# Kernel optimization log

Measured on AMD Instinct MI355X. Metric: run time of the kernel, lower is better.

The kernel has to match this reference:

```python
import jax, jax.numpy as jnp
import numpy as np

N = 131072      # 8192 sudoku puzzles x 16 cells
E = 1048576     # random constraint edges (avg degree 8)
HID = 64
NEG_SLOPE = 0.2


def setup_inputs() -> dict:
    key = jax.random.key(0)
    ks = jax.random.split(key, 18)
    p = lambda k, shape: jax.random.normal(k, shape, dtype=jnp.float32) * 0.05
    return {
        "x": jax.random.randint(ks[0], (N,), 0, 5),
        "edge_index": jax.random.randint(ks[1], (2, E), 0, N),
        "emb": p(ks[2], (5, HID)),
        # conv1: in 64 -> heads=4, C=64, concat
        "W1": p(ks[3], (HID, 4 * HID)),
        "a1_src": p(ks[4], (4, HID)),
        "a1_dst": p(ks[5], (4, HID)),
        "b1": p(ks[6], (4 * HID,)),
        # conv2: in 256 -> heads=4, C=64, concat
        "W2": p(ks[7], (4 * HID, 4 * HID)),
        "a2_src": p(ks[8], (4, HID)),
        "a2_dst": p(ks[9], (4, HID)),
        "b2": p(ks[10], (4 * HID,)),
        # conv3: in 256 -> heads=1, C=64, no concat
        "W3": p(ks[11], (4 * HID, HID)),
        "a3_src": p(ks[12], (1, HID)),
        "a3_dst": p(ks[13], (1, HID)),
        "b3": p(ks[14], (HID,)),
        "fc_w": p(ks[15], (HID, 5)),
        "fc_b": p(ks[16], (5,)),
    }


def gat_conv(x, src, dst, W, a_src, a_dst, b, concat):
    """PyG-style GATConv (self-loops already appended to src/dst)."""
    n = x.shape[0]
    H, C = a_src.shape
    h = (x @ W).reshape(n, H, C)                       # [N,H,C]
    alpha_s = jnp.einsum('nhc,hc->nh', h, a_src)       # [N,H]
    alpha_d = jnp.einsum('nhc,hc->nh', h, a_dst)
    e = jax.nn.leaky_relu(alpha_s[src] + alpha_d[dst], NEG_SLOPE)  # [E,H]
    # scatter-softmax over incoming edges per destination node
    e_max = jax.ops.segment_max(e, dst, num_segments=n)
    e_exp = jnp.exp(e - e_max[dst])
    denom = jax.ops.segment_sum(e_exp, dst, num_segments=n)
    alpha = e_exp / (denom[dst] + 1e-16)               # [E,H]
    msg = h[src] * alpha[:, :, None]                   # [E,H,C]
    out = jax.ops.segment_sum(msg, dst, num_segments=n)  # [N,H,C]
    out = out.reshape(n, H * C) if concat else out.mean(axis=1)
    return out + b


def reference(x, edge_index, emb, W1, a1_src, a1_dst, b1,
              W2, a2_src, a2_dst, b2, W3, a3_src, a3_dst, b3, fc_w, fc_b):
    n = x.shape[0]
    loops = jnp.arange(n)
    src = jnp.concatenate([edge_index[0], loops])  # add self-loops (PyG default)
    dst = jnp.concatenate([edge_index[1], loops])
    h = emb[x]                                                    # [N,64]
    h = jax.nn.elu(gat_conv(h, src, dst, W1, a1_src, a1_dst, b1, True))
    h = jax.nn.elu(gat_conv(h, src, dst, W2, a2_src, a2_dst, b2, True))
    h = jax.nn.elu(gat_conv(h, src, dst, W3, a3_src, a3_dst, b3, False))
    return h @ fc_w + fc_b                                        # [N,5]
```

## Files before the change

### kernel.cpp

```cpp
#include <hip/hip_runtime.h>
#include <hip/hip_bf16.h>
#include <hip/hip_fp8.h>

typedef __attribute__((ext_vector_type(8))) short short8;
typedef __attribute__((ext_vector_type(4))) short short4_t;
typedef __attribute__((ext_vector_type(4))) float floatx4;
typedef __attribute__((ext_vector_type(2))) float floatx2;

constexpr int NB  = 256;
constexpr int CAP = 6144;

__device__ __forceinline__ unsigned short f2bf(float f){
  unsigned int u = __float_as_uint(f);
  u += 0x7FFF + ((u >> 16) & 1);
  return (unsigned short)(u >> 16);
}
__device__ __forceinline__ float bf2f(unsigned short h){
  return __uint_as_float(((unsigned int)h) << 16);
}
__device__ __forceinline__ float lrelu(float x){ return x > 0.f ? x : 0.2f * x; }
__device__ __forceinline__ float eluf(float x){ return x > 0.f ? x : (__expf(x) - 1.f); }

__device__ __forceinline__ unsigned char f2fp8(float f){
  __hip_fp8_e4m3 t(f);
  return (unsigned char)t.__x;
}
__device__ __forceinline__ float fp82f(unsigned char b){
  __hip_fp8_e4m3 t;
  t.__x = (__hip_fp8_storage_t)b;
  return (float)t;
}

template<bool HI>
__device__ __forceinline__ floatx2 fp8pk2(unsigned int v){
#if defined(__has_builtin) && __has_builtin(__builtin_amdgcn_cvt_pk_f32_fp8)
  return __builtin_amdgcn_cvt_pk_f32_fp8((int)v, HI);
#else
  floatx2 r;
  constexpr int sh = HI ? 16 : 0;
  r.x = fp82f((unsigned char)((v >> sh) & 0xFF));
  r.y = fp82f((unsigned char)((v >> (sh + 8)) & 0xFF));
  return r;
#endif
}

__device__ __forceinline__ unsigned int f32x4_to_fp8(float a0, float a1, float a2, float a3){
#if defined(__has_builtin) && __has_builtin(__builtin_amdgcn_cvt_pk_fp8_f32)
  int w = 0;
  w = __builtin_amdgcn_cvt_pk_fp8_f32(a0, a1, w, false);
  w = __builtin_amdgcn_cvt_pk_fp8_f32(a2, a3, w, true);
  return (unsigned int)w;
#else
  return (unsigned int)f2fp8(a0) | ((unsigned int)f2fp8(a1) << 8) |
         ((unsigned int)f2fp8(a2) << 16) | ((unsigned int)f2fp8(a3) << 24);
#endif
}

__device__ __forceinline__ void gload16(const unsigned short* g, unsigned short* l){
  __builtin_amdgcn_global_load_lds(
      (const __attribute__((address_space(1))) unsigned int*)(const void*)g,
      (__attribute__((address_space(3))) unsigned int*)(void*)l,
      16, 0, 0);
}

__global__ __launch_bounds__(256) void part_prep_k(const int* __restrict__ ei, int E, int shift,
                                                   int* __restrict__ gcnt,
                                                   uint2* __restrict__ bbuf, int PB,
                                                   const float* __restrict__ W2,
                                                   unsigned short* __restrict__ Wp2,
                                                   const float* __restrict__ W3,
                                                   unsigned short* __restrict__ Wp3,
                                                   const float* __restrict__ emb,
                                                   const float* __restrict__ W1,
                                                   const float* __restrict__ a1s,
                                                   const float* __restrict__ a1d,
                                                   float* __restrict__ T1,
                                                   float* __restrict__ wt_tab){
  int blk = blockIdx.x;
  int tid = threadIdx.x;
  if (blk < PB){
    __shared__ int hist[NB];
    __shared__ int base[NB];
    hist[tid] = 0;
    __syncthreads();
    int blk_start = blk * 4096;
    int src[16], bkt[16], lp[16];
    #pragma unroll
    for (int k = 0; k < 16; k++){
      int i = blk_start + k * 256 + tid;
      if (i < E){
        int dst = ei[E + i];
        src[k] = ei[i];
        bkt[k] = dst >> shift;
        lp[k] = atomicAdd(&hist[bkt[k]], 1);
      } else {
        bkt[k] = -1;
      }
    }
    __syncthreads();
    base[tid] = atomicAdd(&gcnt[tid], hist[tid]);
    __syncthreads();
    #pragma unroll
    for (int k = 0; k < 16; k++){
      int i = blk_start + k * 256 + tid;
      if (i < E){
        int b = bkt[k];
        int dst = ei[E + i];
        bbuf[(size_t)b * CAP + base[b] + lp[k]] = make_uint2((unsigned)src[k], (unsigned)dst);
      }
    }
    return;
  }
  int b = blk - PB;
  if (b < 256){
    int idx = b * 256 + tid;
    int k = idx >> 8, nn = idx & 255;
    Wp2[nn * 256 + k] = f2bf(W2[idx]);
  } else if (b < 320){
    int idx = (b - 256) * 256 + tid;
    int k = idx >> 6, nn = idx & 63;
    Wp3[nn * 256 + k] = f2bf(W3[idx]);
  } else {
    __shared__ float t_lds[1280];
    __shared__ float as_l[20], ad_l[20];
    for (int i = tid; i < 1280; i += 256){
      int r = i >> 8, c = i & 255;
      float s = 0.f;
      for (int k = 0; k < 64; k++) s += emb[r * 64 + k] * W1[k * 256 + c];
      t_lds[i] = s;
      T1[i] = s;
    }
    __syncthreads();
    if (tid < 20){
      int r = tid >> 2, hh = tid & 3;
      float ss = 0.f, sd = 0.f;
      for (int c = 0; c < 64; c++){
        float f = t_lds[r * 256 + hh * 64 + c];
        ss += f * a1s[hh * 64 + c];
        sd += f * a1d[hh * 64 + c];
      }
      as_l[tid] = ss;
      ad_l[tid] = sd;
    }
    __syncthreads();
    if (tid < 100){
      int xd = tid / 20, rest = tid % 20;
      int h = rest & 3;
      wt_tab[tid] = __expf(lrelu(as_l[rest] + ad_l[xd * 4 + h]));
    }
  }
}

__global__ __launch_bounds__(256) void bscan_k(const int* __restrict__ gcnt,
                                               int* __restrict__ gbase,
                                               int* __restrict__ row_ptr, int N, int dpb){
  __shared__ int s[NB];
  int t = threadIdx.x;
  int v = gcnt[t] + dpb;
  s[t] = v;
  __syncthreads();
  #pragma unroll
  for (int off = 1; off < NB; off <<= 1){
    int u = (t >= off) ? s[t - off] : 0;
    __syncthreads();
    s[t] += u;
    __syncthreads();
  }
  gbase[t] = s[t] - v;
  if (t == NB - 1){ gbase[NB] = s[t]; row_ptr[N] = s[t]; }
}

__global__ __launch_bounds__(256) void sort_k(const uint2* __restrict__ bbuf,
                                              const int* __restrict__ gcnt,
                                              const int* __restrict__ gbase,
                                              int* __restrict__ row_ptr,
                                              int* __restrict__ sorted_src, int dpb){
  __shared__ int counts[512];
  __shared__ int curs[512];
  __shared__ int wsum[256];
  __shared__ int sortedL[CAP + 512];
  int b = blockIdx.x, tid = threadIdx.x;
  int cnt = gcnt[b];
  int dstBase = b * dpb;
  int gb = gbase[b];
  counts[tid] = 0;
  counts[tid + 256] = 0;
  __syncthreads();
  for (int i = tid; i < cnt; i += 256){
    uint2 p = bbuf[(size_t)b * CAP + i];
    atomicAdd(&counts[(int)p.y - dstBase], 1);
  }
  __syncthreads();
  int c0 = counts[2 * tid] + 1;
  int c1 = counts[2 * tid + 1] + 1;
  int sum = c0 + c1;
  wsum[tid] = sum;
  __syncthreads();
  #pragma unroll
  for (int off = 1; off < 256; off <<= 1){
    int u = (tid >= off) ? wsum[tid - off] : 0;
    __syncthreads();
    wsum[tid] += u;
    __syncthreads();
  }
  int ex = wsum[tid] - sum;
  int ro0 = ex, ro1 = ex + c0;
  curs[2 * tid] = ro0 + 1;
  curs[2 * tid + 1] = ro1 + 1;
  sortedL[ro0] = dstBase + 2 * tid;
  sortedL[ro1] = dstBase + 2 * tid + 1;
  row_ptr[dstBase + 2 * tid] = gb + ro0;
  row_ptr[dstBase + 2 * tid + 1] = gb + ro1;
  __syncthreads();
  for (int i = tid; i < cnt; i += 256){
    uint2 p = bbuf[(size_t)b * CAP + i];
    int pos = atomicAdd(&curs[(int)p.y - dstBase], 1);
    sortedL[pos] = (int)p.x;
  }
  __syncthreads();
  int tot = cnt + dpb;
  for (int i = tid; i < tot; i += 256) sorted_src[gb + i] = sortedL[i];
}

template<int BN, int MODE, bool F8OUT>
__global__ __launch_bounds__(256) void gemm_lds_k(const unsigned short* __restrict__ A,
                                                  const unsigned short* __restrict__ Wp,
                                                  void* __restrict__ Cout, int Nc,
                                                  const float* __restrict__ a_src,
                                                  const float* __restrict__ a_dst,
                                                  float* __restrict__ as_arr,
                                                  float* __restrict__ ad_arr){
  constexpr int K = 256;
  constexpr int NT = BN / 32;
  __shared__ unsigned short Alds[128 * 32];
  __shared__ unsigned short Blds[BN * 32];
  __shared__ float asl[128], adl[128];
  __shared__ float pas[128][2], pad[128][2];
  int tid = threadIdx.x;
  int w = tid >> 6, l = tid & 63;
  int r16 = l & 15, quad = l >> 4;
  int wr = w >> 1, wc = w & 1;
  int mBase = blockIdx.x * 128;
  int nBase = blockIdx.y * BN;

  if constexpr (MODE == 1){
    if (tid < 128){ asl[tid] = a_src[nBase + tid]; adl[tid] = a_dst[nBase + tid]; }
  }
  if constexpr (MODE == 2){
    if (tid < 64){ asl[tid] = a_src[tid]; adl[tid] = a_dst[tid]; }
  }

  int arow = l >> 2;
  int kcol = (l & 3) * 8;
  const unsigned short* gA0 = A + (size_t)(mBase + w * 32 + arow) * K + kcol;
  const unsigned short* gA1 = gA0 + (size_t)16 * K;
  unsigned short* lA0 = &Alds[(w * 32) * 32];
  unsigned short* lA1 = &Alds[(w * 32 + 16) * 32];
  const unsigned short* gB0;
  const unsigned short* gB1 = nullptr;
  unsigned short* lB0;
  unsigned short* lB1 = nullptr;
  if constexpr (BN == 128){
    gB0 = Wp + (size_t)(nBase + w * 32 + arow) * K + kcol;
    gB1 = gB0 + (size_t)16 * K;
    lB0 = &Blds[(w * 32) * 32];
    lB1 = &Blds[(w * 32 + 16) * 32];
  } else {
    gB0 = Wp + (size_t)(nBase + w * 16 + arow) * K + kcol;
    lB0 = &Blds[(w * 16) * 32];
  }

  floatx4 acc[4][NT];
  #pragma unroll
  for (int mt = 0; mt < 4; mt++)
    #pragma unroll
    for (int nt = 0; nt < NT; nt++){ floatx4 z = {0.f,0.f,0.f,0.f}; acc[mt][nt] = z; }

  for (int kt = 0; kt < 8; kt++){
    int ko = kt * 32;
    gload16(gA0 + ko, lA0);
    gload16(gA1 + ko, lA1);
    gload16(gB0 + ko, lB0);
    if constexpr (BN == 128) gload16(gB1 + ko, lB1);
    __syncthreads();
    short8 af[4], bfr[NT];
    #pragma unroll
    for (int mt = 0; mt < 4; mt++)
      af[mt] = *(const short8*)&Alds[(wr * 64 + mt * 16 + r16) * 32 + quad * 8];
    #pragma unroll
    for (int nt = 0; nt < NT; nt++)
      bfr[nt] = *(const short8*)&Blds[(wc * (BN / 2) + nt * 16 + r16) * 32 + quad * 8];
    #pragma unroll
    for (int mt = 0; mt < 4; mt++)
      #pragma unroll
      for (int nt = 0; nt < NT; nt++)
        acc[mt][nt] = __builtin_amdgcn_mfma_f32_16x16x32_bf16(af[mt], bfr[nt], acc[mt][nt], 0, 0, 0);
    __syncthreads();
  }

  #pragma unroll
  for (int mt = 0; mt < 4; mt++){
    #pragma unroll
    for (int nt = 0; nt < NT; nt++){
      if constexpr (F8OUT){
        unsigned int pk = f32x4_to_fp8(acc[mt][nt][0] * 64.f, acc[mt][nt][1] * 64.f,
                                       acc[mt][nt][2] * 64.f, acc[mt][nt][3] * 64.f);
        int col = nBase + wc * (BN / 2) + nt * 16 + r16;
        int row0 = mBase + wr * 64 + mt * 16 + quad * 4;
        #pragma unroll
        for (int r = 0; r < 4; r++)
          ((unsigned char*)Cout)[(size_t)(row0 + r) * Nc + col] =
              (unsigned char)((pk >> (r * 8)) & 0xFF);
      } else {
        #pragma unroll
        for (int r = 0; r < 4; r++){
          int row = mBase + wr * 64 + mt * 16 + quad * 4 + r;
          int col = nBase + wc * (BN / 2) + nt * 16 + r16;
          ((unsigned short*)Cout)[(size_t)row * Nc + col] = f2bf(acc[mt][nt][r]);
        }
      }
    }
  }
  if constexpr (MODE == 1){
    int head = (nBase + wc * 64) >> 6;
    #pragma unroll
    for (int mt = 0; mt < 4; mt++){
      #pragma unroll
      for (int r = 0; r < 4; r++){
        float ps = 0.f, pd = 0.f;
        #pragma unroll
        for (int nt = 0; nt < NT; nt++){
          float v = acc[mt][nt][r];
          int ci = wc * 64 + nt * 16 + r16;
          ps += v * asl[ci];
          pd += v * adl[ci];
        }
        ps += __shfl_xor(ps, 1, 64); ps += __shfl_xor(ps, 2, 64);
        ps += __shfl_xor(ps, 4, 64); ps += __shfl_xor(ps, 8, 64);
        pd += __shfl_xor(pd, 1, 64); pd += __shfl_xor(pd, 2, 64);
        pd += __shfl_xor(pd, 4, 64); pd += __shfl_xor(pd, 8, 64);
        if (r16 == 0){
          int row = mBase + wr * 64 + mt * 16 + quad * 4 + r;
          as_arr[row * 4 + head] = ps;
          ad_arr[row * 4 + head] = pd;
        }
      }
    }
  }
  if constexpr (MODE == 2){
    #pragma unroll
    for (int mt = 0; mt < 4; mt++){
      #pragma unroll
      for (int r = 0; r < 4; r++){
        float ps = 0.f, pd = 0.f;
        #pragma unroll
        for (int nt = 0; nt < NT; nt++){
          float v = acc[mt][nt][r];
          int ci = wc * 32 + nt * 16 + r16;
          ps += v * asl[ci];
          pd += v * adl[ci];
        }
        ps += __shfl_xor(ps, 1, 64); ps += __shfl_xor(ps, 2, 64);
        ps += __shfl_xor(ps, 4, 64); ps += __shfl_xor(ps, 8, 64);
        pd += __shfl_xor(pd, 1, 64); pd += __shfl_xor(pd, 2, 64);
        pd += __shfl_xor(pd, 4, 64); pd += __shfl_xor(pd, 8, 64);
        if (r16 == 0){
          int lr = wr * 64 + mt * 16 + quad * 4 + r;
          pas[lr][wc] = ps;
          pad[lr][wc] = pd;
        }
      }
    }
    __syncthreads();
    if (tid < 128){
      as_arr[mBase + tid] = pas[tid][0] + pas[tid][1];
      ad_arr[mBase + tid] = pad[tid][0] + pad[tid][1];
    }
  }
}


__global__ __launch_bounds__(256) void agg1_k(const int* __restrict__ x,
                                              const float* __restrict__ T1,
                                              const float* __restrict__ wt_tab,
                                              const int* __restrict__ row_ptr,
                                              const int* __restrict__ sorted_src,
                                              const float* __restrict__ bias,
                                              unsigned short* __restrict__ outb){
  __shared__ float t_lds[1280];
  __shared__ float wt_l[100], b_lds[256];
  __shared__ float cnt_lds[256][5];
  __shared__ int xd_lds[256];
  int tid = threadIdx.x;
  for (int i = tid; i < 1280; i += 256) t_lds[i] = T1[i];
  if (tid < 100) wt_l[tid] = wt_tab[tid];
  b_lds[tid] = bias[tid];
  int d = blockIdx.x * 256 + tid;
  int start = row_ptr[d], end = row_ptr[d + 1];
  xd_lds[tid] = x[d];
  float c0 = 0.f, c1 = 0.f, c2 = 0.f, c3 = 0.f, c4 = 0.f;
  for (int e = start; e < end; e++){
    int xs = x[sorted_src[e]];
    c0 += (xs == 0) ? 1.f : 0.f;
    c1 += (xs == 1) ? 1.f : 0.f;
    c2 += (xs == 2) ? 1.f : 0.f;
    c3 += (xs == 3) ? 1.f : 0.f;
    c4 += (xs == 4) ? 1.f : 0.f;
  }
  cnt_lds[tid][0] = c0; cnt_lds[tid][1] = c1; cnt_lds[tid][2] = c2;
  cnt_lds[tid][3] = c3; cnt_lds[tid][4] = c4;
  __syncthreads();
  int w = tid >> 6, l = tid & 63;
  int head = l >> 4;
  int c0i = l * 4;
  for (int dl = w; dl < 256; dl += 4){
    int dd = blockIdx.x * 256 + dl;
    int xd20 = xd_lds[dl] * 20;
    float ws[5];
    float den = 0.f;
    #pragma unroll
    for (int v2 = 0; v2 < 5; v2++){
      float wv = wt_l[xd20 + v2 * 4 + head] * cnt_lds[dl][v2];
      ws[v2] = wv;
      den += wv;
    }
    float inv = 1.f / (den + 1e-16f);
    float num[4] = {0.f, 0.f, 0.f, 0.f};
    #pragma unroll
    for (int v2 = 0; v2 < 5; v2++){
      const float4 row = *(const float4*)&t_lds[v2 * 256 + c0i];
      num[0] += ws[v2] * row.x;
      num[1] += ws[v2] * row.y;
      num[2] += ws[v2] * row.z;
      num[3] += ws[v2] * row.w;
    }
    short4_t ov;
    #pragma unroll
    for (int j = 0; j < 4; j++)
      ov[j] = (short)f2bf(eluf(num[j] * inv + b_lds[c0i + j]));
    *(short4_t*)(outb + (size_t)dd * 256 + c0i) = ov;
  }
}


__global__ __launch_bounds__(256) void agg4_k(const unsigned char* __restrict__ h8,
                                              const float* __restrict__ as_arr,
                                              const float* __restrict__ ad_arr,
                                              const int* __restrict__ row_ptr,
                                              const int* __restrict__ sorted_src,
                                              const float* __restrict__ bias,
                                              unsigned short* __restrict__ outb){
  __shared__ float b_lds[256];
  int tid = threadIdx.x;
  b_lds[tid] = bias[tid];
  __syncthreads();
  int w = tid >> 6, l = tid & 63;
  int d = blockIdx.x * 4 + w;
  int hl = l & 31, half = l >> 5;
  unsigned head = (unsigned)(hl >> 3);
  unsigned hloff = (unsigned)(hl * 8);
  int start = row_ptr[d], end = row_ptr[d + 1];
  float a_d = ad_arr[d * 4 + head];
  floatx2 ac0 = {0.f, 0.f}, ac1 = {0.f, 0.f}, ac2 = {0.f, 0.f}, ac3 = {0.f, 0.f};
  float den = 0.f;
  int e = start + half;
  for (; e + 6 < end; e += 8){
    unsigned sA = (unsigned)sorted_src[e];
    unsigned sB = (unsigned)sorted_src[e + 2];
    unsigned sC = (unsigned)sorted_src[e + 4];
    unsigned sD = (unsigned)sorted_src[e + 6];
    uint2 vA = *(const uint2*)(h8 + ((sA << 8) | hloff));
    uint2 vB = *(const uint2*)(h8 + ((sB << 8) | hloff));
    uint2 vC = *(const uint2*)(h8 + ((sC << 8) | hloff));
    uint2 vD = *(const uint2*)(h8 + ((sD << 8) | hloff));
    float wgA = __expf(lrelu(as_arr[(sA << 2) + head] + a_d));
    float wgB = __expf(lrelu(as_arr[(sB << 2) + head] + a_d));
    float wgC = __expf(lrelu(as_arr[(sC << 2) + head] + a_d));
    float wgD = __expf(lrelu(as_arr[(sD << 2) + head] + a_d));
    den += (wgA + wgB) + (wgC + wgD);
    floatx2 wA = {wgA, wgA}, wB = {wgB, wgB}, wC = {wgC, wgC}, wD = {wgD, wgD};
    ac0 += wA * fp8pk2<false>(vA.x) + wB * fp8pk2<false>(vB.x)
         + wC * fp8pk2<false>(vC.x) + wD * fp8pk2<false>(vD.x);
    ac1 += wA * fp8pk2<true>(vA.x)  + wB * fp8pk2<true>(vB.x)
         + wC * fp8pk2<true>(vC.x)  + wD * fp8pk2<true>(vD.x);
    ac2 += wA * fp8pk2<false>(vA.y) + wB * fp8pk2<false>(vB.y)
         + wC * fp8pk2<false>(vC.y) + wD * fp8pk2<false>(vD.y);
    ac3 += wA * fp8pk2<true>(vA.y)  + wB * fp8pk2<true>(vB.y)
         + wC * fp8pk2<true>(vC.y)  + wD * fp8pk2<true>(vD.y);
  }
  for (; e + 2 < end; e += 4){
    unsigned sA = (unsigned)sorted_src[e];
    unsigned sB = (unsigned)sorted_src[e + 2];
    uint2 vA = *(const uint2*)(h8 + ((sA << 8) | hloff));
    uint2 vB = *(const uint2*)(h8 + ((sB << 8) | hloff));
    float wgA = __expf(lrelu(as_arr[(sA << 2) + head] + a_d));
    float wgB = __expf(lrelu(as_arr[(sB << 2) + head] + a_d));
    den += wgA + wgB;
    floatx2 wA = {wgA, wgA}, wB = {wgB, wgB};
    ac0 += wA * fp8pk2<false>(vA.x) + wB * fp8pk2<false>(vB.x);
    ac1 += wA * fp8pk2<true>(vA.x)  + wB * fp8pk2<true>(vB.x);
    ac2 += wA * fp8pk2<false>(vA.y) + wB * fp8pk2<false>(vB.y);
    ac3 += wA * fp8pk2<true>(vA.y)  + wB * fp8pk2<true>(vB.y);
  }
  for (; e < end; e += 2){
    unsigned s = (unsigned)sorted_src[e];
    float wg = __expf(lrelu(as_arr[(s << 2) + head] + a_d));
    den += wg;
    uint2 v = *(const uint2*)(h8 + ((s << 8) | hloff));
    floatx2 wv = {wg, wg};
    ac0 += wv * fp8pk2<false>(v.x);
    ac1 += wv * fp8pk2<true>(v.x);
    ac2 += wv * fp8pk2<false>(v.y);
    ac3 += wv * fp8pk2<true>(v.y);
  }
  float acc[8] = {ac0.x, ac0.y, ac1.x, ac1.y, ac2.x, ac2.y, ac3.x, ac3.y};
  #pragma unroll
  for (int j = 0; j < 8; j++) acc[j] += __shfl_xor(acc[j], 32, 64);
  den += __shfl_xor(den, 32, 64);
  if (half == 0){
    float inv = 0.015625f / (den + 1e-16f);
    short8 ov;
    #pragma unroll
    for (int j = 0; j < 8; j++){
      float v = eluf(acc[j] * inv + b_lds[hl * 8 + j]);
      ov[j] = (short)f2bf(v);
    }
    *(short8*)(outb + (size_t)d * 256 + hl * 8) = ov;
  }
}


__global__ __launch_bounds__(256) void agg3_k(const unsigned char* __restrict__ h8,
                                              const float* __restrict__ as_arr,
                                              const float* __restrict__ ad_arr,
                                              const int* __restrict__ row_ptr,
                                              const int* __restrict__ sorted_src,
                                              const float* __restrict__ bias,
                                              unsigned short* __restrict__ outb){
  __shared__ float b_lds[64];
  int tid = threadIdx.x;
  if (tid < 64) b_lds[tid] = bias[tid];
  __syncthreads();
  int w = tid >> 6, l = tid & 63;
  int d = blockIdx.x * 4 + w;
  int q = l & 7, grp = l >> 3;
  unsigned qoff = (unsigned)(q * 8);
  int start = row_ptr[d], end = row_ptr[d + 1];
  float a_d = ad_arr[d];
  floatx2 ac0 = {0.f, 0.f}, ac1 = {0.f, 0.f}, ac2 = {0.f, 0.f}, ac3 = {0.f, 0.f};
  float den = 0.f;
  int e = start + grp;
  for (; e + 8 < end; e += 16){
    unsigned sA = (unsigned)sorted_src[e];
    unsigned sB = (unsigned)sorted_src[e + 8];
    uint2 vA = *(const uint2*)(h8 + ((sA << 6) | qoff));
    uint2 vB = *(const uint2*)(h8 + ((sB << 6) | qoff));
    float wgA = __expf(lrelu(as_arr[sA] + a_d));
    float wgB = __expf(lrelu(as_arr[sB] + a_d));
    den += wgA + wgB;
    floatx2 wA = {wgA, wgA}, wB = {wgB, wgB};
    ac0 += wA * fp8pk2<false>(vA.x) + wB * fp8pk2<false>(vB.x);
    ac1 += wA * fp8pk2<true>(vA.x)  + wB * fp8pk2<true>(vB.x);
    ac2 += wA * fp8pk2<false>(vA.y) + wB * fp8pk2<false>(vB.y);
    ac3 += wA * fp8pk2<true>(vA.y)  + wB * fp8pk2<true>(vB.y);
  }
  for (; e < end; e += 8){
    unsigned s = (unsigned)sorted_src[e];
    float wg = __expf(lrelu(as_arr[s] + a_d));
    den += wg;
    uint2 v = *(const uint2*)(h8 + ((s << 6) | qoff));
    floatx2 wv = {wg, wg};
    ac0 += wv * fp8pk2<false>(v.x);
    ac1 += wv * fp8pk2<true>(v.x);
    ac2 += wv * fp8pk2<false>(v.y);
    ac3 += wv * fp8pk2<true>(v.y);
  }
  float acc[8] = {ac0.x, ac0.y, ac1.x, ac1.y, ac2.x, ac2.y, ac3.x, ac3.y};
  #pragma unroll
  for (int j = 0; j < 8; j++){
    acc[j] += __shfl_xor(acc[j], 8, 64);
    acc[j] += __shfl_xor(acc[j], 16, 64);
    acc[j] += __shfl_xor(acc[j], 32, 64);
  }
  den += __shfl_xor(den, 8, 64);
  den += __shfl_xor(den, 16, 64);
  den += __shfl_xor(den, 32, 64);
  if (l < 8){
    float inv = 0.015625f / (den + 1e-16f);
    short8 ov;
    #pragma unroll
    for (int j = 0; j < 8; j++){
      float v = eluf(acc[j] * inv + b_lds[q * 8 + j]);
      ov[j] = (short)f2bf(v);
    }
    *(short8*)(outb + (size_t)d * 64 + q * 8) = ov;
  }
}


__global__ __launch_bounds__(256) void fc_k(const unsigned short* __restrict__ hb,
                                            const float* __restrict__ fcw,
                                            const float* __restrict__ fcb,
                                            float* __restrict__ out){
  __shared__ float w_lds[320];
  __shared__ float b_lds[5];
  int tid = threadIdx.x;
  for (int i = tid; i < 320; i += 256) w_lds[i] = fcw[i];
  if (tid < 5) b_lds[tid] = fcb[tid];
  __syncthreads();
  int n = blockIdx.x * 256 + tid;
  const short8* p = (const short8*)(hb + (size_t)n * 64);
  float acc[5];
  #pragma unroll
  for (int j = 0; j < 5; j++) acc[j] = b_lds[j];
  #pragma unroll
  for (int b = 0; b < 8; b++){
    short8 v = p[b];
    #pragma unroll
    for (int j8 = 0; j8 < 8; j8++){
      float f = bf2f((unsigned short)v[j8]);
      int k = b * 8 + j8;
      #pragma unroll
      for (int j = 0; j < 5; j++) acc[j] += f * w_lds[k * 5 + j];
    }
  }
  #pragma unroll
  for (int j = 0; j < 5; j++) out[(size_t)n * 5 + j] = acc[j];
}


extern "C" void kernel_launch(void* const* d_in, const int* in_sizes, int n_in,
                              void* d_out, int out_size, void* d_ws, size_t ws_size,
                              hipStream_t stream){
  const int*   x    = (const int*)d_in[0];
  const int*   ei   = (const int*)d_in[1];
  const float* emb  = (const float*)d_in[2];
  const float* W1   = (const float*)d_in[3];
  const float* a1s  = (const float*)d_in[4];
  const float* a1d  = (const float*)d_in[5];
  const float* b1   = (const float*)d_in[6];
  const float* W2   = (const float*)d_in[7];
  const float* a2s  = (const float*)d_in[8];
  const float* a2d  = (const float*)d_in[9];
  const float* b2   = (const float*)d_in[10];
  const float* W3   = (const float*)d_in[11];
  const float* a3s  = (const float*)d_in[12];
  const float* a3d  = (const float*)d_in[13];
  const float* b3   = (const float*)d_in[14];
  const float* fcw  = (const float*)d_in[15];
  const float* fcb  = (const float*)d_in[16];
  float* out = (float*)d_out;

  const int N = in_sizes[0];
  const int E = in_sizes[1] / 2;
  const int dpb = N / NB;
  int shift = 0;
  while ((1 << shift) < dpb) shift++;
  const int PB = (E + 4095) / 4096;

  char* base = (char*)d_ws;
  size_t off = 0;
  auto alloc = [&](size_t bytes) -> void* {
    void* p = base + off;
    off += (bytes + 255) & ~(size_t)255;
    return p;
  };
  unsigned short* bufB    = (unsigned short*)alloc((size_t)N * 256 * 2);
  unsigned char*  buf8    = (unsigned char*)alloc((size_t)N * 256);
  float* alpha_s          = (float*)alloc((size_t)N * 4 * 4);
  float* alpha_d          = (float*)alloc((size_t)N * 4 * 4);
  int* row_ptr            = (int*)alloc((size_t)(N + 1) * 4);
  int* sorted_src         = (int*)alloc((size_t)(E + N) * 4);
  uint2* bbuf             = (uint2*)alloc((size_t)NB * CAP * 8);
  int* gcnt               = (int*)alloc((size_t)NB * 4);
  int* gbase              = (int*)alloc((size_t)(NB + 1) * 4);
  float* T1               = (float*)alloc(5 * 256 * 4);
  float* wt_tab           = (float*)alloc(100 * 4);
  unsigned short* Wp2     = (unsigned short*)alloc(256 * 256 * 2);
  unsigned short* Wp3     = (unsigned short*)alloc(64 * 256 * 2);

  (void)hipMemsetAsync(gcnt, 0, (size_t)NB * 4, stream);
  part_prep_k<<<PB + 321, 256, 0, stream>>>(ei, E, shift, gcnt, bbuf, PB,
                                            W2, Wp2, W3, Wp3, emb, W1, a1s, a1d, T1, wt_tab);
  bscan_k<<<1, 256, 0, stream>>>(gcnt, gbase, row_ptr, N, dpb);
  sort_k<<<NB, 256, 0, stream>>>(bbuf, gcnt, gbase, row_ptr, sorted_src, dpb);

  agg1_k<<<N / 256, 256, 0, stream>>>(x, T1, wt_tab, row_ptr, sorted_src, b1, bufB);

  gemm_lds_k<128, 1, true><<<dim3(N / 128, 2), 256, 0, stream>>>(bufB, Wp2, buf8, 256,
                                                                 a2s, a2d, alpha_s, alpha_d);
  agg4_k<<<N / 4, 256, 0, stream>>>(buf8, alpha_s, alpha_d, row_ptr, sorted_src, b2, bufB);

  gemm_lds_k<64, 2, true><<<dim3(N / 128, 1), 256, 0, stream>>>(bufB, Wp3, buf8, 64,
                                                                a3s, a3d, alpha_s, alpha_d);
  agg3_k<<<N / 4, 256, 0, stream>>>(buf8, alpha_s, alpha_d, row_ptr, sorted_src, b3, bufB);

  fc_k<<<N / 256, 256, 0, stream>>>(bufB, fcw, fcb, out);
}
```

Before: 352.6 us.

## Degree-sort nodes per bucket and pack multiple destinations per wavefront in aggregation

The sort kernel now builds a per-bucket permutation that orders destination nodes by in-degree (capped at 63) using a small LDS histogram. The aggregation kernels follow this permutation so that lanes working on nodes of similar degree share a wavefront, which limits divergence. agg4 and agg3 now give each destination 16 or 8 lanes instead of a whole wavefront, with each lane handling wider feature slices and walking the edges serially, which removes the cross-lane shuffle reductions. The trade-off is that each lane runs a longer serial edge loop, destination writes become scattered, and sort_k does extra work including a serial scan on one thread.

```diff
diff --git a/kernel.cpp b/kernel.cpp
--- a/kernel.cpp
+++ b/kernel.cpp
@@ -174,11 +174,13 @@
                                               const int* __restrict__ gcnt,
                                               const int* __restrict__ gbase,
                                               int* __restrict__ row_ptr,
-                                              int* __restrict__ sorted_src, int dpb){
+                                              int* __restrict__ sorted_src,
+                                              int* __restrict__ perm, int dpb){
   __shared__ int counts[512];
   __shared__ int curs[512];
   __shared__ int wsum[256];
   __shared__ int sortedL[CAP + 512];
+  __shared__ int dh[64];
   int b = blockIdx.x, tid = threadIdx.x;
   int cnt = gcnt[b];
   int dstBase = b * dpb;
@@ -220,6 +222,22 @@
   __syncthreads();
   int tot = cnt + dpb;
   for (int i = tid; i < tot; i += 256) sorted_src[gb + i] = sortedL[i];
+
+  __syncthreads();
+  if (tid < 64) dh[tid] = 0;
+  __syncthreads();
+  int dg0 = c0 < 63 ? c0 : 63;
+  int dg1 = c1 < 63 ? c1 : 63;
+  int r0 = atomicAdd(&dh[dg0], 1);
+  int r1 = atomicAdd(&dh[dg1], 1);
+  __syncthreads();
+  if (tid == 0){
+    int run = 0;
+    for (int i = 0; i < 64; i++){ int c = dh[i]; dh[i] = run; run += c; }
+  }
+  __syncthreads();
+  perm[dstBase + dh[dg0] + r0] = dstBase + 2 * tid;
+  perm[dstBase + dh[dg1] + r1] = dstBase + 2 * tid + 1;
 }
 
 template<int BN, int MODE, bool F8OUT>
@@ -385,19 +403,22 @@
                                               const float* __restrict__ wt_tab,
                                               const int* __restrict__ row_ptr,
                                               const int* __restrict__ sorted_src,
+                                              const int* __restrict__ perm,
                                               const float* __restrict__ bias,
                                               unsigned short* __restrict__ outb){
   __shared__ float t_lds[1280];
   __shared__ float wt_l[100], b_lds[256];
   __shared__ float cnt_lds[256][5];
   __shared__ int xd_lds[256];
+  __shared__ int dd_lds[256];
   int tid = threadIdx.x;
   for (int i = tid; i < 1280; i += 256) t_lds[i] = T1[i];
   if (tid < 100) wt_l[tid] = wt_tab[tid];
   b_lds[tid] = bias[tid];
-  int d = blockIdx.x * 256 + tid;
+  int d = perm[blockIdx.x * 256 + tid];
   int start = row_ptr[d], end = row_ptr[d + 1];
   xd_lds[tid] = x[d];
+  dd_lds[tid] = d;
   float c0 = 0.f, c1 = 0.f, c2 = 0.f, c3 = 0.f, c4 = 0.f;
   for (int e = start; e < end; e++){
     int xs = x[sorted_src[e]];
@@ -414,7 +435,7 @@
   int head = l >> 4;
   int c0i = l * 4;
   for (int dl = w; dl < 256; dl += 4){
-    int dd = blockIdx.x * 256 + dl;
+    int dd = dd_lds[dl];
     int xd20 = xd_lds[dl] * 20;
     float ws[5];
     float den = 0.f;
@@ -448,6 +469,7 @@
                                               const float* __restrict__ ad_arr,
                                               const int* __restrict__ row_ptr,
                                               const int* __restrict__ sorted_src,
+                                              const int* __restrict__ perm,
                                               const float* __restrict__ bias,
                                               unsigned short* __restrict__ outb){
   __shared__ float b_lds[256];
@@ -455,78 +477,65 @@
   b_lds[tid] = bias[tid];
   __syncthreads();
   int w = tid >> 6, l = tid & 63;
-  int d = blockIdx.x * 4 + w;
-  int hl = l & 31, half = l >> 5;
-  unsigned head = (unsigned)(hl >> 3);
-  unsigned hloff = (unsigned)(hl * 8);
+  int g = l >> 4, q = l & 15;
+  int d = perm[blockIdx.x * 16 + w * 4 + g];
+  unsigned coff = (unsigned)(q * 16);
+  int head = q >> 2;
   int start = row_ptr[d], end = row_ptr[d + 1];
   float a_d = ad_arr[d * 4 + head];
-  floatx2 ac0 = {0.f, 0.f}, ac1 = {0.f, 0.f}, ac2 = {0.f, 0.f}, ac3 = {0.f, 0.f};
+  floatx2 ac[8];
+  #pragma unroll
+  for (int j = 0; j < 8; j++){ floatx2 z = {0.f, 0.f}; ac[j] = z; }
   float den = 0.f;
-  int e = start + half;
-  for (; e + 6 < end; e += 8){
+  int e = start;
+  for (; e + 1 < end; e += 2){
     unsigned sA = (unsigned)sorted_src[e];
-    unsigned sB = (unsigned)sorted_src[e + 2];
-    unsigned sC = (unsigned)sorted_src[e + 4];
-    unsigned sD = (unsigned)sorted_src[e + 6];
-    uint2 vA = *(const uint2*)(h8 + ((sA << 8) | hloff));
-    uint2 vB = *(const uint2*)(h8 + ((sB << 8) | hloff));
-    uint2 vC = *(const uint2*)(h8 + ((sC << 8) | hloff));
-    uint2 vD = *(const uint2*)(h8 + ((sD << 8) | hloff));
-    float wgA = __expf(lrelu(as_arr[(sA << 2) + head] + a_d));
-    float wgB = __expf(lrelu(as_arr[(sB << 2) + head] + a_d));
-    float wgC = __expf(lrelu(as_arr[(sC << 2) + head] + a_d));
-    float wgD = __expf(lrelu(as_arr[(sD << 2) + head] + a_d));
-    den += (wgA + wgB) + (wgC + wgD);
-    floatx2 wA = {wgA, wgA}, wB = {wgB, wgB}, wC = {wgC, wgC}, wD = {wgD, wgD};
-    ac0 += wA * fp8pk2<false>(vA.x) + wB * fp8pk2<false>(vB.x)
-         + wC * fp8pk2<false>(vC.x) + wD * fp8pk2<false>(vD.x);
-    ac1 += wA * fp8pk2<true>(vA.x)  + wB * fp8pk2<true>(vB.x)
-         + wC * fp8pk2<true>(vC.x)  + wD * fp8pk2<true>(vD.x);
-    ac2 += wA * fp8pk2<false>(vA.y) + wB * fp8pk2<false>(vB.y)
-         + wC * fp8pk2<false>(vC.y) + wD * fp8pk2<false>(vD.y);
-    ac3 += wA * fp8pk2<true>(vA.y)  + wB * fp8pk2<true>(vB.y)
-         + wC * fp8pk2<true>(vC.y)  + wD * fp8pk2<true>(vD.y);
-  }
-  for (; e + 2 < end; e += 4){
-    unsigned sA = (unsigned)sorted_src[e];
-    unsigned sB = (unsigned)sorted_src[e + 2];
-    uint2 vA = *(const uint2*)(h8 + ((sA << 8) | hloff));
-    uint2 vB = *(const uint2*)(h8 + ((sB << 8) | hloff));
+    unsigned sB = (unsigned)sorted_src[e + 1];
+    uint4 vA = *(const uint4*)(h8 + (((size_t)sA << 8) | coff));
+    uint4 vB = *(const uint4*)(h8 + (((size_t)sB << 8) | coff));
     float wgA = __expf(lrelu(as_arr[(sA << 2) + head] + a_d));
     float wgB = __expf(lrelu(as_arr[(sB << 2) + head] + a_d));
     den += wgA + wgB;
     floatx2 wA = {wgA, wgA}, wB = {wgB, wgB};
-    ac0 += wA * fp8pk2<false>(vA.x) + wB * fp8pk2<false>(vB.x);
-    ac1 += wA * fp8pk2<true>(vA.x)  + wB * fp8pk2<true>(vB.x);
-    ac2 += wA * fp8pk2<false>(vA.y) + wB * fp8pk2<false>(vB.y);
-    ac3 += wA * fp8pk2<true>(vA.y)  + wB * fp8pk2<true>(vB.y);
-  }
-  for (; e < end; e += 2){
+    ac[0] += wA * fp8pk2<false>(vA.x) + wB * fp8pk2<false>(vB.x);
+    ac[1] += wA * fp8pk2<true>(vA.x)  + wB * fp8pk2<true>(vB.x);
+    ac[2] += wA * fp8pk2<false>(vA.y) + wB * fp8pk2<false>(vB.y);
+    ac[3] += wA * fp8pk2<true>(vA.y)  + wB * fp8pk2<true>(vB.y);
+    ac[4] += wA * fp8pk2<false>(vA.z) + wB * fp8pk2<false>(vB.z);
+    ac[5] += wA * fp8pk2<true>(vA.z)  + wB * fp8pk2<true>(vB.z);
+    ac[6] += wA * fp8pk2<false>(vA.w) + wB * fp8pk2<false>(vB.w);
+    ac[7] += wA * fp8pk2<true>(vA.w)  + wB * fp8pk2<true>(vB.w);
+  }
+  if (e < end){
     unsigned s = (unsigned)sorted_src[e];
+    uint4 v = *(const uint4*)(h8 + (((size_t)s << 8) | coff));
     float wg = __expf(lrelu(as_arr[(s << 2) + head] + a_d));
     den += wg;
-    uint2 v = *(const uint2*)(h8 + ((s << 8) | hloff));
     floatx2 wv = {wg, wg};
-    ac0 += wv * fp8pk2<false>(v.x);
-    ac1 += wv * fp8pk2<true>(v.x);
-    ac2 += wv * fp8pk2<false>(v.y);
-    ac3 += wv * fp8pk2<true>(v.y);
-  }
-  float acc[8] = {ac0.x, ac0.y, ac1.x, ac1.y, ac2.x, ac2.y, ac3.x, ac3.y};
-  #pragma unroll
-  for (int j = 0; j < 8; j++) acc[j] += __shfl_xor(acc[j], 32, 64);
-  den += __shfl_xor(den, 32, 64);
-  if (half == 0){
-    float inv = 0.015625f / (den + 1e-16f);
-    short8 ov;
-    #pragma unroll
-    for (int j = 0; j < 8; j++){
-      float v = eluf(acc[j] * inv + b_lds[hl * 8 + j]);
-      ov[j] = (short)f2bf(v);
-    }
-    *(short8*)(outb + (size_t)d * 256 + hl * 8) = ov;
-  }
+    ac[0] += wv * fp8pk2<false>(v.x);
+    ac[1] += wv * fp8pk2<true>(v.x);
+    ac[2] += wv * fp8pk2<false>(v.y);
+    ac[3] += wv * fp8pk2<true>(v.y);
+    ac[4] += wv * fp8pk2<false>(v.z);
+    ac[5] += wv * fp8pk2<true>(v.z);
+    ac[6] += wv * fp8pk2<false>(v.w);
+    ac[7] += wv * fp8pk2<true>(v.w);
+  }
+  float inv = 0.015625f / (den + 1e-16f);
+  int cb = q * 16;
+  short8 o0, o1;
+  #pragma unroll
+  for (int j = 0; j < 8; j++){
+    float v = ((j & 1) ? ac[j >> 1].y : ac[j >> 1].x);
+    o0[j] = (short)f2bf(eluf(v * inv + b_lds[cb + j]));
+  }
+  #pragma unroll
+  for (int j = 0; j < 8; j++){
+    float v = ((j & 1) ? ac[4 + (j >> 1)].y : ac[4 + (j >> 1)].x);
+    o1[j] = (short)f2bf(eluf(v * inv + b_lds[cb + 8 + j]));
+  }
+  *(short8*)(outb + (size_t)d * 256 + cb) = o0;
+  *(short8*)(outb + (size_t)d * 256 + cb + 8) = o1;
 }
 
 
@@ -535,6 +544,7 @@
                                               const float* __restrict__ ad_arr,
                                               const int* __restrict__ row_ptr,
                                               const int* __restrict__ sorted_src,
+                                              const int* __restrict__ perm,
                                               const float* __restrict__ bias,
                                               unsigned short* __restrict__ outb){
   __shared__ float b_lds[64];
@@ -542,59 +552,50 @@
   if (tid < 64) b_lds[tid] = bias[tid];
   __syncthreads();
   int w = tid >> 6, l = tid & 63;
-  int d = blockIdx.x * 4 + w;
-  int q = l & 7, grp = l >> 3;
-  unsigned qoff = (unsigned)(q * 8);
+  int g = l >> 3, q = l & 7;
+  int d = perm[blockIdx.x * 32 + w * 8 + g];
+  unsigned coff = (unsigned)(q * 8);
   int start = row_ptr[d], end = row_ptr[d + 1];
   float a_d = ad_arr[d];
-  floatx2 ac0 = {0.f, 0.f}, ac1 = {0.f, 0.f}, ac2 = {0.f, 0.f}, ac3 = {0.f, 0.f};
+  floatx2 ac[4];
+  #pragma unroll
+  for (int j = 0; j < 4; j++){ floatx2 z = {0.f, 0.f}; ac[j] = z; }
   float den = 0.f;
-  int e = start + grp;
-  for (; e + 8 < end; e += 16){
+  int e = start;
+  for (; e + 1 < end; e += 2){
     unsigned sA = (unsigned)sorted_src[e];
-    unsigned sB = (unsigned)sorted_src[e + 8];
-    uint2 vA = *(const uint2*)(h8 + ((sA << 6) | qoff));
-    uint2 vB = *(const uint2*)(h8 + ((sB << 6) | qoff));
+    unsigned sB = (unsigned)sorted_src[e + 1];
+    uint2 vA = *(const uint2*)(h8 + (((size_t)sA << 6) | coff));
+    uint2 vB = *(const uint2*)(h8 + (((size_t)sB << 6) | coff));
     float wgA = __expf(lrelu(as_arr[sA] + a_d));
     float wgB = __expf(lrelu(as_arr[sB] + a_d));
     den += wgA + wgB;
     floatx2 wA = {wgA, wgA}, wB = {wgB, wgB};
-    ac0 += wA * fp8pk2<false>(vA.x) + wB * fp8pk2<false>(vB.x);
-    ac1 += wA * fp8pk2<true>(vA.x)  + wB * fp8pk2<true>(vB.x);
-    ac2 += wA * fp8pk2<false>(vA.y) + wB * fp8pk2<false>(vB.y);
-    ac3 += wA * fp8pk2<true>(vA.y)  + wB * fp8pk2<true>(vB.y);
-  }
-  for (; e < end; e += 8){
+    ac[0] += wA * fp8pk2<false>(vA.x) + wB * fp8pk2<false>(vB.x);
+    ac[1] += wA * fp8pk2<true>(vA.x)  + wB * fp8pk2<true>(vB.x);
+    ac[2] += wA * fp8pk2<false>(vA.y) + wB * fp8pk2<false>(vB.y);
+    ac[3] += wA * fp8pk2<true>(vA.y)  + wB * fp8pk2<true>(vB.y);
+  }
+  if (e < end){
     unsigned s = (unsigned)sorted_src[e];
     float wg = __expf(lrelu(as_arr[s] + a_d));
     den += wg;
-    uint2 v = *(const uint2*)(h8 + ((s << 6) | qoff));
+    uint2 v = *(const uint2*)(h8 + (((size_t)s << 6) | coff));
     floatx2 wv = {wg, wg};
-    ac0 += wv * fp8pk2<false>(v.x);
-    ac1 += wv * fp8pk2<true>(v.x);
-    ac2 += wv * fp8pk2<false>(v.y);
-    ac3 += wv * fp8pk2<true>(v.y);
-  }
-  float acc[8] = {ac0.x, ac0.y, ac1.x, ac1.y, ac2.x, ac2.y, ac3.x, ac3.y};
+    ac[0] += wv * fp8pk2<false>(v.x);
+    ac[1] += wv * fp8pk2<true>(v.x);
+    ac[2] += wv * fp8pk2<false>(v.y);
+    ac[3] += wv * fp8pk2<true>(v.y);
+  }
+  float inv = 0.015625f / (den + 1e-16f);
+  int cb = q * 8;
+  short8 ov;
   #pragma unroll
   for (int j = 0; j < 8; j++){
-    acc[j] += __shfl_xor(acc[j], 8, 64);
-    acc[j] += __shfl_xor(acc[j], 16, 64);
-    acc[j] += __shfl_xor(acc[j], 32, 64);
-  }
-  den += __shfl_xor(den, 8, 64);
-  den += __shfl_xor(den, 16, 64);
-  den += __shfl_xor(den, 32, 64);
-  if (l < 8){
-    float inv = 0.015625f / (den + 1e-16f);
-    short8 ov;
-    #pragma unroll
-    for (int j = 0; j < 8; j++){
-      float v = eluf(acc[j] * inv + b_lds[q * 8 + j]);
-      ov[j] = (short)f2bf(v);
-    }
-    *(short8*)(outb + (size_t)d * 64 + q * 8) = ov;
-  }
+    float v = ((j & 1) ? ac[j >> 1].y : ac[j >> 1].x);
+    ov[j] = (short)f2bf(eluf(v * inv + b_lds[cb + j]));
+  }
+  *(short8*)(outb + (size_t)d * 64 + cb) = ov;
 }
 
 
@@ -671,6 +672,7 @@
   float* alpha_d          = (float*)alloc((size_t)N * 4 * 4);
   int* row_ptr            = (int*)alloc((size_t)(N + 1) * 4);
   int* sorted_src         = (int*)alloc((size_t)(E + N) * 4);
+  int* perm               = (int*)alloc((size_t)N * 4);
   uint2* bbuf             = (uint2*)alloc((size_t)NB * CAP * 8);
   int* gcnt               = (int*)alloc((size_t)NB * 4);
   int* gbase              = (int*)alloc((size_t)(NB + 1) * 4);
@@ -683,17 +685,17 @@
   part_prep_k<<<PB + 321, 256, 0, stream>>>(ei, E, shift, gcnt, bbuf, PB,
                                             W2, Wp2, W3, Wp3, emb, W1, a1s, a1d, T1, wt_tab);
   bscan_k<<<1, 256, 0, stream>>>(gcnt, gbase, row_ptr, N, dpb);
-  sort_k<<<NB, 256, 0, stream>>>(bbuf, gcnt, gbase, row_ptr, sorted_src, dpb);
-
-  agg1_k<<<N / 256, 256, 0, stream>>>(x, T1, wt_tab, row_ptr, sorted_src, b1, bufB);
+  sort_k<<<NB, 256, 0, stream>>>(bbuf, gcnt, gbase, row_ptr, sorted_src, perm, dpb);
+
+  agg1_k<<<N / 256, 256, 0, stream>>>(x, T1, wt_tab, row_ptr, sorted_src, perm, b1, bufB);
 
   gemm_lds_k<128, 1, true><<<dim3(N / 128, 2), 256, 0, stream>>>(bufB, Wp2, buf8, 256,
                                                                  a2s, a2d, alpha_s, alpha_d);
-  agg4_k<<<N / 4, 256, 0, stream>>>(buf8, alpha_s, alpha_d, row_ptr, sorted_src, b2, bufB);
+  agg4_k<<<N / 16, 256, 0, stream>>>(buf8, alpha_s, alpha_d, row_ptr, sorted_src, perm, b2, bufB);
 
   gemm_lds_k<64, 2, true><<<dim3(N / 128, 1), 256, 0, stream>>>(bufB, Wp3, buf8, 64,
                                                                 a3s, a3d, alpha_s, alpha_d);
-  agg3_k<<<N / 4, 256, 0, stream>>>(buf8, alpha_s, alpha_d, row_ptr, sorted_src, b3, bufB);
+  agg3_k<<<N / 32, 256, 0, stream>>>(buf8, alpha_s, alpha_d, row_ptr, sorted_src, perm, b3, bufB);
 
   fc_k<<<N / 256, 256, 0, stream>>>(bufB, fcw, fcb, out);
 }
```

Result: faster. 344.8 us (-2.2%).
